# Kernel tuning notes

Hardware: AMD Instinct MI355X
Metric: run time of the kernel (lower is better)

The kernel has to match this reference:

```python
import jax, jax.numpy as jnp
import numpy as np

N, D, K = 8192, 256, 8          # batch, feat dim, instances per class
MARGIN1, MARGIN2 = 0.0, 0.7


def setup_inputs() -> dict:
    key = jax.random.key(0)
    inputs = jax.random.normal(key, (N, D), dtype=jnp.float32)
    # classes appear in contiguous blocks of K, as the k_size loop assumes
    targets = jnp.arange(N, dtype=jnp.int32) // K
    return {"inputs": inputs, "targets": targets}


def reference(inputs, targets):
    n = inputs.shape[0]
    num_classes = n // K

    # l2-normalize features
    x = inputs / jnp.linalg.norm(inputs, axis=1, keepdims=True)

    # per-class centers (segment mean), then gather back per sample
    sums = jax.ops.segment_sum(x, targets, num_segments=num_classes)           # [C, D]
    counts = jax.ops.segment_sum(jnp.ones((n, 1), x.dtype), targets,
                                 num_segments=num_classes)                     # [C, 1]
    class_centers = sums / counts
    centers = class_centers[targets]                                           # [N, D]

    # sample-to-center distance (uses normalized centers)
    centers_n = centers / jnp.linalg.norm(centers, axis=1, keepdims=True)
    dist_pc = jnp.sqrt(jnp.sum((x - centers_n) ** 2, axis=1))                  # [N]
    dist_pc = jnp.maximum(dist_pc - MARGIN1, 0.0)

    # pairwise distances between (unnormalized) per-sample centers
    sq = jnp.sum(centers ** 2, axis=1)                                         # [N]
    dist = sq[:, None] + sq[None, :] - 2.0 * (centers @ centers.T)             # [N, N]
    dist = jnp.sqrt(jnp.maximum(dist, 1e-12))

    # one anchor per k_size block: masked mean of hinge over negatives
    anchors = jnp.arange(0, n, K)                                              # [N//K]
    rows = dist[anchors]                                                       # [N//K, N]
    neg = (targets[anchors][:, None] != targets[None, :]).astype(dist.dtype)   # [N//K, N]
    vals = jnp.maximum(MARGIN2 - rows, 0.0) * neg
    dist_an = jnp.sum(vals, axis=1) / jnp.sum(neg, axis=1)                     # [N//K]

    dist_pc_mean = dist_pc.mean()
    dist_an_mean = dist_an.mean()
    loss = dist_pc_mean + dist_an_mean
    return (loss, dist_pc_mean, dist_an_mean)
```

## Files before the change

kernel.cpp:

```cpp
#include <hip/hip_runtime.h>

#define NN 8192
#define DD 256
#define KK 8
#define CC 1024
#define RS 2048
#define M2 0.7f
#define TILE 64
#define KC 32


__device__ inline float wsum(float v) {
#pragma unroll
    for (int m = 1; m < 64; m <<= 1) v += __shfl_xor(v, m, 64);
    return v;
}

__global__ __launch_bounds__(64) void centers_kernel(
    const float* x, float* cc, int cstr, float* sq, int sqstr, float* acc) {
    const int c = blockIdx.x;
    const int lane = threadIdx.x;
    const float* base = x + (size_t)c * RS + 4 * lane;

    float4 v[KK];
#pragma unroll
    for (int r = 0; r < KK; ++r) v[r] = *(const float4*)(base + r * DD);

    float rw[KK];
    float cx = 0.f, cy = 0.f, cz = 0.f, cw = 0.f;
#pragma unroll
    for (int r = 0; r < KK; ++r) {
        const float s = wsum(v[r].x * v[r].x + v[r].y * v[r].y +
                             v[r].z * v[r].z + v[r].w * v[r].w);
        rw[r] = rsqrtf(s);
        cx += v[r].x * rw[r]; cy += v[r].y * rw[r];
        cz += v[r].z * rw[r]; cw += v[r].w * rw[r];
    }
    cx *= 0.125f; cy *= 0.125f; cz *= 0.125f; cw *= 0.125f;

    float4 cvec = make_float4(cx, cy, cz, cw);
    *(float4*)(cc + (size_t)c * cstr + 4 * lane) = cvec;

    const float ssc = wsum(cx * cx + cy * cy + cz * cz + cw * cw);
    if (lane == 0) sq[(size_t)c * sqstr] = ssc;
    const float rn = rsqrtf(ssc);
    const float nx = cx * rn, ny = cy * rn, nz = cz * rn, nw = cw * rn;

    float pc = 0.0f;
#pragma unroll
    for (int r = 0; r < KK; ++r) {
        const float dx = v[r].x * rw[r] - nx;
        const float dy = v[r].y * rw[r] - ny;
        const float dz = v[r].z * rw[r] - nz;
        const float dw = v[r].w * rw[r] - nw;
        pc += sqrtf(wsum(dx * dx + dy * dy + dz * dz + dw * dw));
    }
    if (lane == 0) atomicAdd(acc + 0, pc);
}

__global__ __launch_bounds__(256) void pair_kernel(
    const float* __restrict__ cc, int cstr,
    const float* __restrict__ sq, int sqstr,
    float* acc, float* out) {
    __shared__ float As[KC][TILE + 4];
    __shared__ float Bs[KC][TILE + 4];
    __shared__ float sqa_s[TILE], sqc_s[TILE];
    __shared__ float red[4];

    const int tid = threadIdx.x;
    const int tx = tid & 15, ty = tid >> 4;
    const int a0 = blockIdx.y * TILE, c0 = blockIdx.x * TILE;
    const int lrow = tid >> 2;
    const int lq = tid & 3;

    if (tid < 64) sqa_s[tid] = sq[(size_t)(a0 + tid) * sqstr];
    else if (tid < 128) sqc_s[tid - 64] = sq[(size_t)(c0 + tid - 64) * sqstr];

    float dot[4][4] = {};

    for (int kk = 0; kk < DD; kk += KC) {
#pragma unroll
        for (int m = 0; m < 2; ++m) {
            const int q = lq + 4 * m;
            const float4 av = *(const float4*)(cc + (size_t)(a0 + lrow) * cstr + kk + 4 * q);
            const float4 bv = *(const float4*)(cc + (size_t)(c0 + lrow) * cstr + kk + 4 * q);
            As[4 * q + 0][lrow] = av.x; As[4 * q + 1][lrow] = av.y;
            As[4 * q + 2][lrow] = av.z; As[4 * q + 3][lrow] = av.w;
            Bs[4 * q + 0][lrow] = bv.x; Bs[4 * q + 1][lrow] = bv.y;
            Bs[4 * q + 2][lrow] = bv.z; Bs[4 * q + 3][lrow] = bv.w;
        }
        __syncthreads();
#pragma unroll
        for (int k = 0; k < KC; ++k) {
            const float4 a4 = *(const float4*)&As[k][4 * ty];
            const float4 b4 = *(const float4*)&Bs[k][4 * tx];
            dot[0][0] += a4.x * b4.x; dot[0][1] += a4.x * b4.y;
            dot[0][2] += a4.x * b4.z; dot[0][3] += a4.x * b4.w;
            dot[1][0] += a4.y * b4.x; dot[1][1] += a4.y * b4.y;
            dot[1][2] += a4.y * b4.z; dot[1][3] += a4.y * b4.w;
            dot[2][0] += a4.z * b4.x; dot[2][1] += a4.z * b4.y;
            dot[2][2] += a4.z * b4.z; dot[2][3] += a4.z * b4.w;
            dot[3][0] += a4.w * b4.x; dot[3][1] += a4.w * b4.y;
            dot[3][2] += a4.w * b4.z; dot[3][3] += a4.w * b4.w;
        }
        __syncthreads();
    }

    float hsum = 0.0f;
#pragma unroll
    for (int u = 0; u < 4; ++u) {
#pragma unroll
        for (int vv = 0; vv < 4; ++vv) {
            const int a = a0 + 4 * ty + u, c = c0 + 4 * tx + vv;
            const float dsq = sqa_s[4 * ty + u] + sqc_s[4 * tx + vv]
                              - 2.0f * dot[u][vv];
            const float dist = sqrtf(fmaxf(dsq, 1e-12f));
            const float h = fmaxf(M2 - dist, 0.0f);
            hsum += (a != c) ? h : 0.0f;
        }
    }

    const float w = wsum(hsum);
    if ((tid & 63) == 0) red[tid >> 6] = w;
    __syncthreads();
    if (tid == 0) {
        atomicAdd(acc + 1, red[0] + red[1] + red[2] + red[3]);
        __threadfence();
        const unsigned tkt = atomicAdd((unsigned*)(acc + 3), 1u);
        if (tkt == 16 * 16 - 1) {
            const float pc_sum = atomicAdd(acc + 0, 0.0f);
            const float an_sum = atomicAdd(acc + 1, 0.0f);
            const float pc_mean = pc_sum / (float)NN;
            const float an_mean =
                an_sum * (float)KK / ((float)(NN - KK) * (float)CC);
            out[0] = pc_mean + an_mean;
            out[1] = pc_mean;
            out[2] = an_mean;
        }
    }
}

extern "C" void kernel_launch(void* const* d_in, const int* in_sizes, int n_in,
                              void* d_out, int out_size, void* d_ws, size_t ws_size,
                              hipStream_t stream) {
    float* x = (float*)d_in[0];
    float* out = (float*)d_out;
    float* ws = (float*)d_ws;

    float *acc, *cc, *sq;
    int cstr, sqstr;
    const size_t need = (size_t)(16 + CC * DD + CC) * sizeof(float);
    if (ws_size >= need) {
        acc = ws; cc = ws + 16; cstr = DD; sq = ws + 16 + CC * DD; sqstr = 1;
    } else {
        acc = ws;
        cc = x; cstr = RS;
        sq = x + DD; sqstr = RS;
    }

    hipMemsetAsync(acc, 0, 4 * sizeof(float), stream);

    centers_kernel<<<CC, 64, 0, stream>>>(x, cc, cstr, sq, sqstr, acc);
    dim3 grid2(CC / TILE, CC / TILE);
    pair_kernel<<<grid2, 256, 0, stream>>>(cc, cstr, sq, sqstr, acc, out);
}
```

Baseline: 94.08 us.

## Fuse centers and pairwise kernels into one persistent kernel with grid barrier

Merges the centers computation and the pairwise hinge GEMM into a single 256-block kernel. A global atomic barrier separates the two phases, and a last-block ticket performs a deterministic final reduction from per-block partial arrays in place of float atomics. This removes one kernel launch and the inter-kernel gap. It relies on all 256 blocks being co-resident, which should hold on this GPU, and it adds barrier spin overhead.

```diff
diff --git a/kernel.cpp b/kernel.cpp
--- a/kernel.cpp
+++ b/kernel.cpp
@@ -8,6 +8,7 @@
 #define M2 0.7f
 #define TILE 64
 #define KC 32
+#define GRID 256
 
 
 __device__ inline float wsum(float v) {
@@ -16,74 +17,87 @@
     return v;
 }
 
-__global__ __launch_bounds__(64) void centers_kernel(
-    const float* x, float* cc, int cstr, float* sq, int sqstr, float* acc) {
-    const int c = blockIdx.x;
-    const int lane = threadIdx.x;
-    const float* base = x + (size_t)c * RS + 4 * lane;
-
-    float4 v[KK];
-#pragma unroll
-    for (int r = 0; r < KK; ++r) v[r] = *(const float4*)(base + r * DD);
-
-    float rw[KK];
-    float cx = 0.f, cy = 0.f, cz = 0.f, cw = 0.f;
-#pragma unroll
-    for (int r = 0; r < KK; ++r) {
-        const float s = wsum(v[r].x * v[r].x + v[r].y * v[r].y +
-                             v[r].z * v[r].z + v[r].w * v[r].w);
-        rw[r] = rsqrtf(s);
-        cx += v[r].x * rw[r]; cy += v[r].y * rw[r];
-        cz += v[r].z * rw[r]; cw += v[r].w * rw[r];
-    }
-    cx *= 0.125f; cy *= 0.125f; cz *= 0.125f; cw *= 0.125f;
-
-    float4 cvec = make_float4(cx, cy, cz, cw);
-    *(float4*)(cc + (size_t)c * cstr + 4 * lane) = cvec;
-
-    const float ssc = wsum(cx * cx + cy * cy + cz * cz + cw * cw);
-    if (lane == 0) sq[(size_t)c * sqstr] = ssc;
-    const float rn = rsqrtf(ssc);
-    const float nx = cx * rn, ny = cy * rn, nz = cz * rn, nw = cw * rn;
-
-    float pc = 0.0f;
-#pragma unroll
-    for (int r = 0; r < KK; ++r) {
-        const float dx = v[r].x * rw[r] - nx;
-        const float dy = v[r].y * rw[r] - ny;
-        const float dz = v[r].z * rw[r] - nz;
-        const float dw = v[r].w * rw[r] - nw;
-        pc += sqrtf(wsum(dx * dx + dy * dy + dz * dz + dw * dw));
-    }
-    if (lane == 0) atomicAdd(acc + 0, pc);
-}
-
-__global__ __launch_bounds__(256) void pair_kernel(
-    const float* __restrict__ cc, int cstr,
-    const float* __restrict__ sq, int sqstr,
-    float* acc, float* out) {
+__global__ __launch_bounds__(256) void fused_kernel(
+    const float* __restrict__ x, float* __restrict__ cc,
+    float* __restrict__ sq, float* __restrict__ pcarr,
+    float* __restrict__ anarr, unsigned* __restrict__ bar,
+    float* __restrict__ out) {
+    const int tid = threadIdx.x;
+    const int w = tid >> 6;
+    const int lane = tid & 63;
+
     __shared__ float As[KC][TILE + 4];
     __shared__ float Bs[KC][TILE + 4];
     __shared__ float sqa_s[TILE], sqc_s[TILE];
-    __shared__ float red[4];
-
-    const int tid = threadIdx.x;
+    __shared__ float red[4], red2[4];
+    __shared__ unsigned tkt_s;
+
+    {
+        const int c = blockIdx.x * 4 + w;
+        const float* base = x + (size_t)c * RS + 4 * lane;
+
+        float4 v[KK];
+#pragma unroll
+        for (int r = 0; r < KK; ++r) v[r] = *(const float4*)(base + r * DD);
+
+        float rw[KK];
+        float cx = 0.f, cy = 0.f, cz = 0.f, cw = 0.f;
+#pragma unroll
+        for (int r = 0; r < KK; ++r) {
+            const float s = wsum(v[r].x * v[r].x + v[r].y * v[r].y +
+                                 v[r].z * v[r].z + v[r].w * v[r].w);
+            rw[r] = rsqrtf(s);
+            cx += v[r].x * rw[r]; cy += v[r].y * rw[r];
+            cz += v[r].z * rw[r]; cw += v[r].w * rw[r];
+        }
+        cx *= 0.125f; cy *= 0.125f; cz *= 0.125f; cw *= 0.125f;
+
+        *(float4*)(cc + (size_t)c * DD + 4 * lane) =
+            make_float4(cx, cy, cz, cw);
+
+        const float ssc = wsum(cx * cx + cy * cy + cz * cz + cw * cw);
+        if (lane == 0) sq[c] = ssc;
+        const float rn = rsqrtf(ssc);
+        const float nx = cx * rn, ny = cy * rn, nz = cz * rn, nw = cw * rn;
+
+        float pc = 0.0f;
+#pragma unroll
+        for (int r = 0; r < KK; ++r) {
+            const float dx = v[r].x * rw[r] - nx;
+            const float dy = v[r].y * rw[r] - ny;
+            const float dz = v[r].z * rw[r] - nz;
+            const float dw = v[r].w * rw[r] - nw;
+            pc += sqrtf(wsum(dx * dx + dy * dy + dz * dz + dw * dw));
+        }
+        if (lane == 0) pcarr[c] = pc;
+    }
+
+    __syncthreads();
+    if (tid == 0) {
+        __hip_atomic_fetch_add(&bar[0], 1u, __ATOMIC_RELEASE,
+                               __HIP_MEMORY_SCOPE_AGENT);
+        while (__hip_atomic_load(&bar[0], __ATOMIC_ACQUIRE,
+                                 __HIP_MEMORY_SCOPE_AGENT) < GRID)
+            __builtin_amdgcn_s_sleep(16);
+    }
+    __syncthreads();
+
+    const int a0 = (blockIdx.x >> 4) * TILE;
+    const int c0 = (blockIdx.x & 15) * TILE;
     const int tx = tid & 15, ty = tid >> 4;
-    const int a0 = blockIdx.y * TILE, c0 = blockIdx.x * TILE;
     const int lrow = tid >> 2;
     const int lq = tid & 3;
 
-    if (tid < 64) sqa_s[tid] = sq[(size_t)(a0 + tid) * sqstr];
-    else if (tid < 128) sqc_s[tid - 64] = sq[(size_t)(c0 + tid - 64) * sqstr];
+    if (tid < 64) sqa_s[tid] = sq[a0 + tid];
+    else if (tid < 128) sqc_s[tid - 64] = sq[c0 + tid - 64];
 
     float dot[4][4] = {};
-
     for (int kk = 0; kk < DD; kk += KC) {
 #pragma unroll
         for (int m = 0; m < 2; ++m) {
             const int q = lq + 4 * m;
-            const float4 av = *(const float4*)(cc + (size_t)(a0 + lrow) * cstr + kk + 4 * q);
-            const float4 bv = *(const float4*)(cc + (size_t)(c0 + lrow) * cstr + kk + 4 * q);
+            const float4 av = *(const float4*)(cc + (size_t)(a0 + lrow) * DD + kk + 4 * q);
+            const float4 bv = *(const float4*)(cc + (size_t)(c0 + lrow) * DD + kk + 4 * q);
             As[4 * q + 0][lrow] = av.x; As[4 * q + 1][lrow] = av.y;
             As[4 * q + 2][lrow] = av.z; As[4 * q + 3][lrow] = av.w;
             Bs[4 * q + 0][lrow] = bv.x; Bs[4 * q + 1][lrow] = bv.y;
@@ -115,19 +129,143 @@
             const float dsq = sqa_s[4 * ty + u] + sqc_s[4 * tx + vv]
                               - 2.0f * dot[u][vv];
             const float dist = sqrtf(fmaxf(dsq, 1e-12f));
-            const float h = fmaxf(M2 - dist, 0.0f);
-            hsum += (a != c) ? h : 0.0f;
-        }
-    }
-
-    const float w = wsum(hsum);
-    if ((tid & 63) == 0) red[tid >> 6] = w;
+            hsum += (a != c) ? fmaxf(M2 - dist, 0.0f) : 0.0f;
+        }
+    }
+    {
+        const float s = wsum(hsum);
+        if (lane == 0) red[w] = s;
+    }
+    __syncthreads();
+
+    if (tid == 0) {
+        anarr[blockIdx.x] = red[0] + red[1] + red[2] + red[3];
+        tkt_s = __hip_atomic_fetch_add(&bar[1], 1u, __ATOMIC_ACQ_REL,
+                                       __HIP_MEMORY_SCOPE_AGENT);
+    }
+    __syncthreads();
+
+    if (tkt_s == GRID - 1) {
+        float pcp = pcarr[tid] + pcarr[tid + 256] +
+                    pcarr[tid + 512] + pcarr[tid + 768];
+        float anp = anarr[tid];
+        const float s1 = wsum(pcp);
+        const float s2 = wsum(anp);
+        if (lane == 0) { red[w] = s1; red2[w] = s2; }
+        __syncthreads();
+        if (tid == 0) {
+            const float pc_sum = red[0] + red[1] + red[2] + red[3];
+            const float an_sum = red2[0] + red2[1] + red2[2] + red2[3];
+            const float pc_mean = pc_sum / (float)NN;
+            const float an_mean =
+                an_sum * (float)KK / ((float)(NN - KK) * (float)CC);
+            out[0] = pc_mean + an_mean;
+            out[1] = pc_mean;
+            out[2] = an_mean;
+        }
+    }
+}
+
+__device__ inline float wave_reduce_sum(float v) {
+#pragma unroll
+    for (int off = 32; off > 0; off >>= 1) v += __shfl_down(v, off, 64);
+    return v;
+}
+
+__global__ __launch_bounds__(64) void centers_kernel_fb(
+    const float* x, float* cc, int cstr, float* sq, int sqstr, float* acc) {
+    const int c = blockIdx.x;
+    const int lane = threadIdx.x;
+    const float* base = x + (size_t)c * RS + 4 * lane;
+    float4 v[KK];
+#pragma unroll
+    for (int r = 0; r < KK; ++r) v[r] = *(const float4*)(base + r * DD);
+    float rw[KK];
+    float cx = 0.f, cy = 0.f, cz = 0.f, cw = 0.f;
+#pragma unroll
+    for (int r = 0; r < KK; ++r) {
+        const float s = wsum(v[r].x * v[r].x + v[r].y * v[r].y +
+                             v[r].z * v[r].z + v[r].w * v[r].w);
+        rw[r] = rsqrtf(s);
+        cx += v[r].x * rw[r]; cy += v[r].y * rw[r];
+        cz += v[r].z * rw[r]; cw += v[r].w * rw[r];
+    }
+    cx *= 0.125f; cy *= 0.125f; cz *= 0.125f; cw *= 0.125f;
+    *(float4*)(cc + (size_t)c * cstr + 4 * lane) = make_float4(cx, cy, cz, cw);
+    const float ssc = wsum(cx * cx + cy * cy + cz * cz + cw * cw);
+    if (lane == 0) sq[(size_t)c * sqstr] = ssc;
+    const float rn = rsqrtf(ssc);
+    float pc = 0.0f;
+#pragma unroll
+    for (int r = 0; r < KK; ++r) {
+        const float dx = v[r].x * rw[r] - cx * rn;
+        const float dy = v[r].y * rw[r] - cy * rn;
+        const float dz = v[r].z * rw[r] - cz * rn;
+        const float dw = v[r].w * rw[r] - cw * rn;
+        pc += sqrtf(wsum(dx * dx + dy * dy + dz * dz + dw * dw));
+    }
+    if (lane == 0) atomicAdd(acc + 0, pc);
+}
+
+__global__ __launch_bounds__(256) void pair_kernel_fb(
+    const float* cc, int cstr, const float* sq, int sqstr,
+    float* acc, float* out) {
+    __shared__ float As[KC][TILE + 4];
+    __shared__ float Bs[KC][TILE + 4];
+    __shared__ float sqa_s[TILE], sqc_s[TILE];
+    __shared__ float red[4];
+    const int tid = threadIdx.x;
+    const int tx = tid & 15, ty = tid >> 4;
+    const int a0 = blockIdx.y * TILE, c0 = blockIdx.x * TILE;
+    const int lrow = tid >> 2, lq = tid & 3;
+    if (tid < 64) sqa_s[tid] = sq[(size_t)(a0 + tid) * sqstr];
+    else if (tid < 128) sqc_s[tid - 64] = sq[(size_t)(c0 + tid - 64) * sqstr];
+    float dot[4][4] = {};
+    for (int kk = 0; kk < DD; kk += KC) {
+#pragma unroll
+        for (int m = 0; m < 2; ++m) {
+            const int q = lq + 4 * m;
+            const float4 av = *(const float4*)(cc + (size_t)(a0 + lrow) * cstr + kk + 4 * q);
+            const float4 bv = *(const float4*)(cc + (size_t)(c0 + lrow) * cstr + kk + 4 * q);
+            As[4 * q + 0][lrow] = av.x; As[4 * q + 1][lrow] = av.y;
+            As[4 * q + 2][lrow] = av.z; As[4 * q + 3][lrow] = av.w;
+            Bs[4 * q + 0][lrow] = bv.x; Bs[4 * q + 1][lrow] = bv.y;
+            Bs[4 * q + 2][lrow] = bv.z; Bs[4 * q + 3][lrow] = bv.w;
+        }
+        __syncthreads();
+#pragma unroll
+        for (int k = 0; k < KC; ++k) {
+            const float4 a4 = *(const float4*)&As[k][4 * ty];
+            const float4 b4 = *(const float4*)&Bs[k][4 * tx];
+            dot[0][0] += a4.x * b4.x; dot[0][1] += a4.x * b4.y;
+            dot[0][2] += a4.x * b4.z; dot[0][3] += a4.x * b4.w;
+            dot[1][0] += a4.y * b4.x; dot[1][1] += a4.y * b4.y;
+            dot[1][2] += a4.y * b4.z; dot[1][3] += a4.y * b4.w;
+            dot[2][0] += a4.z * b4.x; dot[2][1] += a4.z * b4.y;
+            dot[2][2] += a4.z * b4.z; dot[2][3] += a4.z * b4.w;
+            dot[3][0] += a4.w * b4.x; dot[3][1] += a4.w * b4.y;
+            dot[3][2] += a4.w * b4.z; dot[3][3] += a4.w * b4.w;
+        }
+        __syncthreads();
+    }
+    float hsum = 0.0f;
+#pragma unroll
+    for (int u = 0; u < 4; ++u)
+#pragma unroll
+        for (int vv = 0; vv < 4; ++vv) {
+            const int a = a0 + 4 * ty + u, c = c0 + 4 * tx + vv;
+            const float dsq = sqa_s[4 * ty + u] + sqc_s[4 * tx + vv]
+                              - 2.0f * dot[u][vv];
+            hsum += (a != c) ? fmaxf(M2 - sqrtf(fmaxf(dsq, 1e-12f)), 0.0f) : 0.0f;
+        }
+    const float s = wsum(hsum);
+    if ((tid & 63) == 0) red[tid >> 6] = s;
     __syncthreads();
     if (tid == 0) {
         atomicAdd(acc + 1, red[0] + red[1] + red[2] + red[3]);
         __threadfence();
         const unsigned tkt = atomicAdd((unsigned*)(acc + 3), 1u);
-        if (tkt == 16 * 16 - 1) {
+        if (tkt == 256 - 1) {
             const float pc_sum = atomicAdd(acc + 0, 0.0f);
             const float an_sum = atomicAdd(acc + 1, 0.0f);
             const float pc_mean = pc_sum / (float)NN;
@@ -147,20 +285,25 @@
     float* out = (float*)d_out;
     float* ws = (float*)d_ws;
 
-    float *acc, *cc, *sq;
-    int cstr, sqstr;
-    const size_t need = (size_t)(16 + CC * DD + CC) * sizeof(float);
+    const size_t need =
+        (size_t)(16 + CC * DD + CC + CC + GRID) * sizeof(float);
+
+    hipMemsetAsync(ws, 0, 64, stream);
+
     if (ws_size >= need) {
-        acc = ws; cc = ws + 16; cstr = DD; sq = ws + 16 + CC * DD; sqstr = 1;
+        unsigned* bar = (unsigned*)ws;
+        float* cc = ws + 16;
+        float* sq = cc + (size_t)CC * DD;
+        float* pcarr = sq + CC;
+        float* anarr = pcarr + CC;
+        fused_kernel<<<GRID, 256, 0, stream>>>(x, cc, sq, pcarr, anarr,
+                                               bar, out);
     } else {
-        acc = ws;
-        cc = x; cstr = RS;
-        sq = x + DD; sqstr = RS;
-    }
-
-    hipMemsetAsync(acc, 0, 4 * sizeof(float), stream);
-
-    centers_kernel<<<CC, 64, 0, stream>>>(x, cc, cstr, sq, sqstr, acc);
-    dim3 grid2(CC / TILE, CC / TILE);
-    pair_kernel<<<grid2, 256, 0, stream>>>(cc, cstr, sq, sqstr, acc, out);
-}
+        float* acc = ws;
+        float* cc = x;  int cstr = RS;
+        float* sq = x + DD; int sqstr = RS;
+        centers_kernel_fb<<<CC, 64, 0, stream>>>(x, cc, cstr, sq, sqstr, acc);
+        dim3 grid2(CC / TILE, CC / TILE);
+        pair_kernel_fb<<<grid2, 256, 0, stream>>>(cc, cstr, sq, sqstr, acc, out);
+    }
+}
```

After: 88.55 us. 5.9% less time.
